# Performance work log

Hardware: AMD Instinct MI355X
Metric: run time of the kernel (lower is better)

The kernel has to match this reference:

```python
import jax, jax.numpy as jnp
import numpy as np

B, T, C = 128, 512, 1024  # batch, time (fixed by `line` buffer), channels


def fft_convolve(a, b):
    """Linear convolution via zero-padded FFT, sliced to a's length.
    a: (1, C, T) kernel, b: (B, C, T) signal. Returns (B, C, T)."""
    n = a.shape[-1]
    a_pad = jnp.pad(a, ((0, 0), (0, 0), (0, n)))
    b_pad = jnp.pad(b, ((0, 0), (0, 0), (0, n)))
    spec = jnp.fft.rfft(a_pad, axis=-1) * jnp.fft.rfft(b_pad, axis=-1)
    return jnp.fft.irfft(spec, n=2 * n, axis=-1)[..., :n]


def setup_inputs() -> dict:
    key = jax.random.key(0)
    k1, k2, k3, k4, k5 = jax.random.split(key, 5)
    bound = 1.0 / np.sqrt(C)  # nn.Linear default init range
    x = jax.random.normal(k1, (B, T, C), dtype=jnp.float32)
    W_proj = jax.random.uniform(k2, (C, C), jnp.float32, -bound, bound)
    W_values = jax.random.uniform(k3, (C, C), jnp.float32, -bound, bound)
    gain = jax.random.uniform(k4, (1, 1, C), jnp.float32, 0.01, 1.0)
    pow_ = jax.random.uniform(k5, (1, C, 1), jnp.float32, -6.0, 6.0)
    line = jnp.linspace(1.0, 0.0, T, dtype=jnp.float32)[None, None, :]  # (1,1,T)
    return {"x": x, "W_proj": W_proj, "W_values": W_values,
            "gain": gain, "pow_": pow_, "line": line}


def reference(x, W_proj, W_values, gain, pow_, line):
    # proj and values (bias-free Linears)
    h = jnp.einsum('btc,dc->btd', x, W_proj)          # (B,T,C)
    v = jnp.einsum('btc,dc->btd', h, W_values)        # (B,T,C)
    # learned power-law kernel, one decay per channel: (1,C,T)
    z = line ** (2.0 + jax.nn.sigmoid(pow_) * 100.0)
    # FFT long convolution along time
    y = fft_convolve(z, jnp.transpose(v, (0, 2, 1)))  # (B,C,T)
    y = jnp.transpose(y, (0, 2, 1))                    # (B,T,C)
    return jax.nn.relu(y * gain)
```

## Files before the change

kernel.cpp:

```cpp
#include <hip/hip_runtime.h>
#include <hip/hip_bf16.h>

#define B_ 128
#define T_ 512
#define C_ 1024

typedef __attribute__((ext_vector_type(8))) short short8;
typedef __attribute__((ext_vector_type(4))) float f32x4;

__device__ __forceinline__ unsigned short f2bf(float f){
  unsigned u; __builtin_memcpy(&u, &f, 4);
  u += 0x7FFFu + ((u >> 16) & 1u);
  return (unsigned short)(u >> 16);
}

typedef __attribute__((address_space(3))) unsigned lds_u32_t;
typedef __attribute__((address_space(1))) unsigned glb_u32_t;
typedef __attribute__((address_space(3))) char lds_char;
__device__ __forceinline__ void gload16(const void* g, void* l){
  __builtin_amdgcn_global_load_lds((const glb_u32_t*)g, (lds_u32_t*)l, 16, 0, 0);
}

__global__ void cast_f32_bf16(const float* __restrict__ in, unsigned short* __restrict__ out, long n){
  long i = (long)blockIdx.x * blockDim.x + threadIdx.x;
  long stride = (long)gridDim.x * blockDim.x;
  for (long j = i * 4; j < n; j += stride * 4){
    float4 v = *(const float4*)(in + j);
    ushort4 o; o.x = f2bf(v.x); o.y = f2bf(v.y); o.z = f2bf(v.z); o.w = f2bf(v.w);
    *(ushort4*)(out + j) = o;
  }
}

__global__ void transpose_cast(const float* __restrict__ in, unsigned short* __restrict__ out){
  __shared__ float tile[32][33];
  int c0 = blockIdx.x * 32, e0 = blockIdx.y * 32;
  int tx = threadIdx.x, ty = threadIdx.y;
  for (int r = 0; r < 32; r += 8)
    tile[ty + r][tx] = in[(size_t)(e0 + ty + r) * C_ + c0 + tx];
  __syncthreads();
  for (int r = 0; r < 32; r += 8)
    out[(size_t)(c0 + ty + r) * C_ + e0 + tx] = f2bf(tile[tx][ty + r]);
}

__global__ __launch_bounds__(256) void gemm_bt_bf16(
    const unsigned short* __restrict__ A,
    const unsigned short* __restrict__ Bt,
    unsigned short* __restrict__ Cc,
    int M, int N, int K)
{
  __shared__ short As[128 * 32];
  __shared__ short Bs[128 * 32];
  const int tid  = threadIdx.x;
  const int lane = tid & 63;
  const int wave = tid >> 6;
  const int wr = wave >> 1, wc = wave & 1;
  const int lr = lane & 15, kg = lane >> 4;
  const int m0 = blockIdx.x * 128;
  const int n0 = blockIdx.y * 128;

  f32x4 acc[4][4];
  #pragma unroll
  for (int mi = 0; mi < 4; mi++)
    #pragma unroll
    for (int ni = 0; ni < 4; ni++)
      acc[mi][ni] = (f32x4){0.f, 0.f, 0.f, 0.f};

  const int r1 = tid >> 2, ch1 = tid & 3;
  char* abase = (char*)As + (tid & ~63) * 16;
  char* bbase = (char*)Bs + (tid & ~63) * 16;

  for (int k0 = 0; k0 < K; k0 += 32){
    __syncthreads();
    gload16(A  + (size_t)(m0 + r1)      * K + k0 + ch1 * 8, abase);
    gload16(A  + (size_t)(m0 + 64 + r1) * K + k0 + ch1 * 8, abase + 4096);
    gload16(Bt + (size_t)(n0 + r1)      * K + k0 + ch1 * 8, bbase);
    gload16(Bt + (size_t)(n0 + 64 + r1) * K + k0 + ch1 * 8, bbase + 4096);
    __syncthreads();

    short8 af[4], bfr[4];
    #pragma unroll
    for (int mi = 0; mi < 4; mi++)
      af[mi] = *(const short8*)&As[(wr * 64 + mi * 16 + lr) * 32 + kg * 8];
    #pragma unroll
    for (int ni = 0; ni < 4; ni++)
      bfr[ni] = *(const short8*)&Bs[(wc * 64 + ni * 16 + lr) * 32 + kg * 8];
    #pragma unroll
    for (int mi = 0; mi < 4; mi++)
      #pragma unroll
      for (int ni = 0; ni < 4; ni++)
        acc[mi][ni] = __builtin_amdgcn_mfma_f32_16x16x32_bf16(af[mi], bfr[ni], acc[mi][ni], 0, 0, 0);
  }

  #pragma unroll
  for (int mi = 0; mi < 4; mi++)
    #pragma unroll
    for (int ni = 0; ni < 4; ni++){
      int n = n0 + wc * 64 + ni * 16 + lr;
      int mb = m0 + wr * 64 + mi * 16 + kg * 4;
      #pragma unroll
      for (int j = 0; j < 4; j++)
        Cc[(size_t)(mb + j) * N + n] = f2bf(acc[mi][ni][j]);
    }
}

#define SWZ(x) ((x) ^ ((((x) >> 7) & 3) << 4))

#define STAGE_A(kt, kh) { \
  int d_ = wv * 1024 + ln * 16; int o_ = SWZ(d_); \
  gload16(Ag + (size_t)(m0 + (o_ >> 6)) * 1024 + (kt) * 64 + (kh) * 32 + ((o_ >> 4) & 3) * 8, \
          ldsc + ((kt) & 1) * 32768 + (kh) * 16384 + wv * 1024); \
  d_ += 8192; o_ = SWZ(d_); \
  gload16(Ag + (size_t)(m0 + (o_ >> 6)) * 1024 + (kt) * 64 + (kh) * 32 + ((o_ >> 4) & 3) * 8, \
          ldsc + ((kt) & 1) * 32768 + (kh) * 16384 + 8192 + wv * 1024); }

#define STAGE_B(kt, kh) { \
  int d_ = wv * 1024 + ln * 16; int o_ = SWZ(d_); \
  gload16(Bg + (size_t)(n0 + (o_ >> 6)) * 1024 + (kt) * 64 + (kh) * 32 + ((o_ >> 4) & 3) * 8, \
          ldsc + 65536 + ((kt) & 1) * 32768 + (kh) * 16384 + wv * 1024); \
  d_ += 8192; o_ = SWZ(d_); \
  gload16(Bg + (size_t)(n0 + (o_ >> 6)) * 1024 + (kt) * 64 + (kh) * 32 + ((o_ >> 4) & 3) * 8, \
          ldsc + 65536 + ((kt) & 1) * 32768 + (kh) * 16384 + 8192 + wv * 1024); }

__global__ __launch_bounds__(512, 2) void gemm256_vt(
    const unsigned short* __restrict__ Ag,
    const unsigned short* __restrict__ Bg,
    unsigned short* __restrict__ vt)
{
  extern __shared__ char ldsc[];
  lds_char* lds3 = (lds_char*)ldsc;
  const int tid = threadIdx.x;
  const int ln  = tid & 63;
  const int wv  = tid >> 6;
  const int wr  = wv >> 2;
  const int wc  = wv & 3;
  const int lr  = ln & 15, kg = ln >> 4;
  const int id  = blockIdx.x;
  const int jj  = (id & 7) * 128 + (id >> 3);
  const int n0  = (jj & 3) * 256;
  const int m0  = (jj >> 2) * 256;

  f32x4 acc[8][4];
  #pragma unroll
  for (int mi = 0; mi < 8; mi++)
    #pragma unroll
    for (int ni = 0; ni < 4; ni++)
      acc[mi][ni] = (f32x4){0.f, 0.f, 0.f, 0.f};

  STAGE_A(0, 0); STAGE_A(0, 1); STAGE_B(0, 0); STAGE_B(0, 1);

  short8 af[2][8], bf2[2][4];

  #pragma unroll 1
  for (int t = 0; t < 16; ++t){
    const int S = t & 1;
    if (t < 15){
      STAGE_A(t + 1, 0); STAGE_A(t + 1, 1); STAGE_B(t + 1, 0); STAGE_B(t + 1, 1);
      __builtin_amdgcn_sched_barrier(0);
      asm volatile("s_waitcnt vmcnt(8)");
      __builtin_amdgcn_sched_barrier(0);
    } else {
      __builtin_amdgcn_sched_barrier(0);
      asm volatile("s_waitcnt vmcnt(0)");
      __builtin_amdgcn_sched_barrier(0);
    }
    __builtin_amdgcn_s_barrier();
    __builtin_amdgcn_sched_barrier(0);

    #pragma unroll
    for (int kk = 0; kk < 2; ++kk){
      #pragma unroll
      for (int mi = 0; mi < 8; mi++){
        int off = S * 32768 + kk * 16384 + (wr * 128 + mi * 16 + lr) * 64 + kg * 16;
        unsigned a_ = (unsigned)(size_t)(lds3 + SWZ(off));
        asm volatile("ds_read_b128 %0, %1" : "=v"(af[kk][mi]) : "v"(a_));
      }
      #pragma unroll
      for (int ni = 0; ni < 4; ni++){
        int off = 65536 + S * 32768 + kk * 16384 + (wc * 64 + ni * 16 + lr) * 64 + kg * 16;
        unsigned a_ = (unsigned)(size_t)(lds3 + SWZ(off));
        asm volatile("ds_read_b128 %0, %1" : "=v"(bf2[kk][ni]) : "v"(a_));
      }
    }

    asm volatile("s_waitcnt lgkmcnt(12)");
    __builtin_amdgcn_sched_barrier(0);
    __builtin_amdgcn_s_setprio(1);
    #pragma unroll
    for (int mi = 0; mi < 8; mi++)
      #pragma unroll
      for (int ni = 0; ni < 4; ni++)
        acc[mi][ni] = __builtin_amdgcn_mfma_f32_16x16x32_bf16(af[0][mi], bf2[0][ni], acc[mi][ni], 0, 0, 0);
    __builtin_amdgcn_s_setprio(0);

    asm volatile("s_waitcnt lgkmcnt(0)");
    __builtin_amdgcn_sched_barrier(0);
    __builtin_amdgcn_s_setprio(1);
    #pragma unroll
    for (int mi = 0; mi < 8; mi++)
      #pragma unroll
      for (int ni = 0; ni < 4; ni++)
        acc[mi][ni] = __builtin_amdgcn_mfma_f32_16x16x32_bf16(af[1][mi], bf2[1][ni], acc[mi][ni], 0, 0, 0);
    __builtin_amdgcn_s_setprio(0);
    __builtin_amdgcn_sched_barrier(0);
    __builtin_amdgcn_s_barrier();
  }

  #pragma unroll
  for (int mi = 0; mi < 8; mi++)
    #pragma unroll
    for (int ni = 0; ni < 4; ni++){
      int n  = n0 + wc * 64 + ni * 16 + lr;
      int mb = m0 + wr * 128 + mi * 16 + kg * 4;
      int bb = mb >> 9, t = mb & 511;
      ushort4 o;
      o.x = f2bf(acc[mi][ni][0]); o.y = f2bf(acc[mi][ni][1]);
      o.z = f2bf(acc[mi][ni][2]); o.w = f2bf(acc[mi][ni][3]);
      *(ushort4*)&vt[((size_t)n * B_ + bb) * T_ + t] = o;
    }
}

__global__ __launch_bounds__(256) void band_prep2(const float* __restrict__ pw,
                                                  const float* __restrict__ line,
                                                  unsigned short* __restrict__ band){
  __shared__ unsigned short zrow[64];
  const int c = blockIdx.x, d32 = blockIdx.y;
  const int tid = threadIdx.x;
  if (tid < 63){
    int k = d32 * 32 - 31 + tid;
    float z = 0.f;
    if (k >= 0 && k < T_){
      float p = pw[c];
      float e = 2.0f + 100.0f / (1.0f + expf(-p));
      float lv = line[k];
      z = (lv > 0.f) ? expf(e * logf(lv)) : 0.f;
    }
    zrow[tid] = f2bf(z);
  }
  __syncthreads();
  const size_t base = ((size_t)c * 16 + d32) * 1280;
  #pragma unroll
  for (int q = 0; q < 5; q++){
    int idx = tid + q * 256;
    int i = idx / 40, j = idx - i * 40;
    unsigned short v = 0;
    if (j < 32){
      int qq = i - j + 31;
      v = zrow[qq];
    }
    band[base + idx] = v;
  }
}

__global__ __launch_bounds__(256) void conv_mfma(
    const unsigned short* __restrict__ vt,
    const unsigned short* __restrict__ band,
    const float* __restrict__ gain,
    unsigned short* __restrict__ Ybf)
{
  __shared__ short Bs[128 * 32];
  __shared__ short Ab[16 * 1280];
  const int id  = blockIdx.x;
  const int xcd = id & 7;
  const int jj  = id >> 3;
  const int c   = xcd + ((jj >> 2) << 3);
  const int t0  = (jj & 3) << 7;
  const int tid = threadIdx.x, lane = tid & 63, wave = tid >> 6;
  const int wr = wave >> 1, wc = wave & 1, lr = lane & 15, kg = lane >> 4;
  const int K  = t0 + 128;
  const int nb = (t0 >> 5) + 4;

  {
    const unsigned short* src = band + (size_t)c * (16 * 1280);
    const int nch = nb * 160;
    for (int q0 = 0; q0 < nch; q0 += 256){
      int q = q0 + tid;
      char* dst = (char*)Ab + q0 * 16 + wave * 1024;
      if (q < nch) gload16(src + (size_t)q * 8, dst);
    }
  }

  f32x4 acc[4][4];
  #pragma unroll
  for (int mi = 0; mi < 4; mi++)
    #pragma unroll
    for (int ni = 0; ni < 4; ni++)
      acc[mi][ni] = (f32x4){0.f, 0.f, 0.f, 0.f};

  const int r1 = tid >> 2, ch1 = tid & 3;
  char* bbase = (char*)Bs + (tid & ~63) * 16;
  const size_t vbase = (size_t)c * B_ * T_;

  for (int k0 = 0; k0 < K; k0 += 32){
    __syncthreads();
    gload16(vt + vbase + (size_t)r1 * T_        + k0 + ch1 * 8, bbase);
    gload16(vt + vbase + (size_t)(64 + r1) * T_ + k0 + ch1 * 8, bbase + 4096);
    __syncthreads();

    short8 bfr[4];
    #pragma unroll
    for (int ni = 0; ni < 4; ni++)
      bfr[ni] = *(const short8*)&Bs[(wc * 64 + ni * 16 + lr) * 32 + kg * 8];

    const int dbase = ((t0 - k0) >> 5) + wr * 2;
    #pragma unroll
    for (int mi = 0; mi < 4; mi++){
      const int d32 = dbase + (mi >> 1);
      if (d32 >= 0){
        const int i = ((mi & 1) << 4) + lr;
        short8 af = *(const short8*)&Ab[d32 * 1280 + i * 40 + kg * 8];
        #pragma unroll
        for (int ni = 0; ni < 4; ni++)
          acc[mi][ni] = __builtin_amdgcn_mfma_f32_16x16x32_bf16(af, bfr[ni], acc[mi][ni], 0, 0, 0);
      }
    }
  }

  const float g = gain[c];
  #pragma unroll
  for (int mi = 0; mi < 4; mi++)
    #pragma unroll
    for (int ni = 0; ni < 4; ni++){
      int t = t0 + wr * 64 + mi * 16 + kg * 4;
      int b = wc * 64 + ni * 16 + lr;
      ushort4 o;
      o.x = f2bf(fmaxf(acc[mi][ni][0] * g, 0.f));
      o.y = f2bf(fmaxf(acc[mi][ni][1] * g, 0.f));
      o.z = f2bf(fmaxf(acc[mi][ni][2] * g, 0.f));
      o.w = f2bf(fmaxf(acc[mi][ni][3] * g, 0.f));
      *(ushort4*)&Ybf[((size_t)c * B_ + b) * T_ + t] = o;
    }
}

__global__ __launch_bounds__(256) void final_out(const unsigned short* __restrict__ Ybf,
                                                 float* __restrict__ out){
  __shared__ unsigned short tile[64][72];
  const int c0 = blockIdx.x * 64;
  const int t0 = blockIdx.y * 64;
  const int b  = blockIdx.z;
  const int tid = threadIdx.x;
  const int cr = tid >> 4;
  const int t4 = (tid & 15) * 4;
  for (int q = 0; q < 64; q += 16){
    ushort4 u = *(const ushort4*)&Ybf[((size_t)(c0 + cr + q) * B_ + b) * T_ + t0 + t4];
    *(ushort4*)&tile[cr + q][t4] = u;
  }
  __syncthreads();
  const int tr = tid >> 4;
  const int c4 = (tid & 15) * 4;
  for (int q = 0; q < 64; q += 16){
    int t = tr + q;
    float4 o;
    o.x = __uint_as_float((unsigned)tile[c4 + 0][t] << 16);
    o.y = __uint_as_float((unsigned)tile[c4 + 1][t] << 16);
    o.z = __uint_as_float((unsigned)tile[c4 + 2][t] << 16);
    o.w = __uint_as_float((unsigned)tile[c4 + 3][t] << 16);
    *(float4*)&out[((size_t)b * T_ + t0 + t) * C_ + c0 + c4] = o;
  }
}

extern "C" void kernel_launch(void* const* d_in, const int* in_sizes, int n_in,
                              void* d_out, int out_size, void* d_ws, size_t ws_size,
                              hipStream_t stream)
{
  (void)in_sizes; (void)n_in; (void)out_size; (void)ws_size;
  const float* x    = (const float*)d_in[0];
  const float* Wp   = (const float*)d_in[1];
  const float* Wv   = (const float*)d_in[2];
  const float* gain = (const float*)d_in[3];
  const float* pw   = (const float*)d_in[4];
  const float* line = (const float*)d_in[5];
  float* out = (float*)d_out;

  char* ws = (char*)d_ws;
  unsigned short* Ybf   = (unsigned short*)ws;
  unsigned short* WpT   = (unsigned short*)(ws + 134217728);
  unsigned short* Wv_bf = (unsigned short*)(ws + 134217728 + 2097152);
  unsigned short* W_f   = (unsigned short*)(ws + 134217728 + 2 * 2097152);
  unsigned short* x_bf  = (unsigned short*)d_out;
  unsigned short* vt    = (unsigned short*)d_out + 67108864;
  unsigned short* bandp = (unsigned short*)d_out;

  cast_f32_bf16<<<256, 256, 0, stream>>>(Wv, Wv_bf, (long)C_ * C_);
  transpose_cast<<<dim3(32, 32), dim3(32, 8), 0, stream>>>(Wp, WpT);
  gemm_bt_bf16<<<dim3(8, 8), 256, 0, stream>>>(Wv_bf, WpT, W_f, C_, C_, C_);
  cast_f32_bf16<<<2048, 256, 0, stream>>>(x, x_bf, (long)B_ * T_ * C_);
  gemm256_vt<<<1024, 512, 131072, stream>>>(x_bf, W_f, vt);
  band_prep2<<<dim3(1024, 16), 256, 0, stream>>>(pw, line, bandp);
  conv_mfma<<<4096, 256, 0, stream>>>(vt, bandp, gain, Ybf);
  final_out<<<dim3(16, 8, 128), 256, 0, stream>>>(Ybf, out);
}
```

Measured before the change: 522.2 us.

## Fuse fp32-to-bf16 cast of x into the main GEMM's A-tile loading

The separate cast kernel for x is removed. The big GEMM now loads fp32 x tiles into registers two steps ahead, converts them to bf16, and writes them to LDS with ds_write, while B is still staged through direct global-to-LDS loads. This saves one full pass writing and re-reading the 128 MB bf16 copy of x. In exchange the GEMM reads twice as many bytes for A, needs more registers, and has a more complex software pipeline in its main loop.

Result: slower. 678.0 us (+29.8%).

```diff
diff --git a/kernel.cpp b/kernel.cpp
--- a/kernel.cpp
+++ b/kernel.cpp
@@ -105,14 +105,6 @@
 
 #define SWZ(x) ((x) ^ ((((x) >> 7) & 3) << 4))
 
-#define STAGE_A(kt, kh) { \
-  int d_ = wv * 1024 + ln * 16; int o_ = SWZ(d_); \
-  gload16(Ag + (size_t)(m0 + (o_ >> 6)) * 1024 + (kt) * 64 + (kh) * 32 + ((o_ >> 4) & 3) * 8, \
-          ldsc + ((kt) & 1) * 32768 + (kh) * 16384 + wv * 1024); \
-  d_ += 8192; o_ = SWZ(d_); \
-  gload16(Ag + (size_t)(m0 + (o_ >> 6)) * 1024 + (kt) * 64 + (kh) * 32 + ((o_ >> 4) & 3) * 8, \
-          ldsc + ((kt) & 1) * 32768 + (kh) * 16384 + 8192 + wv * 1024); }
-
 #define STAGE_B(kt, kh) { \
   int d_ = wv * 1024 + ln * 16; int o_ = SWZ(d_); \
   gload16(Bg + (size_t)(n0 + (o_ >> 6)) * 1024 + (kt) * 64 + (kh) * 32 + ((o_ >> 4) & 3) * 8, \
@@ -121,8 +113,26 @@
   gload16(Bg + (size_t)(n0 + (o_ >> 6)) * 1024 + (kt) * 64 + (kh) * 32 + ((o_ >> 4) & 3) * 8, \
           ldsc + 65536 + ((kt) & 1) * 32768 + (kh) * 16384 + 8192 + wv * 1024); }
 
-__global__ __launch_bounds__(512, 2) void gemm256_vt(
-    const unsigned short* __restrict__ Ag,
+#define LOADA(kt) { \
+  _Pragma("unroll") for (int kh = 0; kh < 2; kh++) \
+    _Pragma("unroll") for (int hf = 0; hf < 2; hf++){ \
+      const float* p_ = Ag32 + (size_t)(m0 + rowA + hf * 128) * 1024 + (kt) * 64 + kh * 32 + c8 * 8; \
+      areg[kh][hf][0] = *(const float4*)p_; \
+      areg[kh][hf][1] = *(const float4*)(p_ + 4); } }
+
+#define CVTWRITE(slot) { \
+  _Pragma("unroll") for (int kh = 0; kh < 2; kh++) \
+    _Pragma("unroll") for (int hf = 0; hf < 2; hf++){ \
+      short8 w_; \
+      _Pragma("unroll") for (int q = 0; q < 4; q++){ \
+        w_[q]     = (short)f2bf(areg[kh][hf][0][q]); \
+        w_[q + 4] = (short)f2bf(areg[kh][hf][1][q]); } \
+      int d_ = wv * 1024 + ln * 16 + hf * 8192; \
+      unsigned ad_ = (unsigned)(size_t)(lds3 + (slot) * 32768 + kh * 16384 + SWZ(d_)); \
+      asm volatile("ds_write_b128 %0, %1" :: "v"(ad_), "v"(w_)); } }
+
+__global__ __launch_bounds__(512, 2) void gemm256_fused(
+    const float* __restrict__ Ag32,
     const unsigned short* __restrict__ Bg,
     unsigned short* __restrict__ vt)
 {
@@ -134,6 +144,8 @@
   const int wr  = wv >> 2;
   const int wc  = wv & 3;
   const int lr  = ln & 15, kg = ln >> 4;
+  const int rowA = wv * 16 + (ln >> 2);
+  const int c8   = ln & 3;
   const int id  = blockIdx.x;
   const int jj  = (id & 7) * 128 + (id >> 3);
   const int n0  = (jj & 3) * 256;
@@ -146,24 +158,28 @@
     for (int ni = 0; ni < 4; ni++)
       acc[mi][ni] = (f32x4){0.f, 0.f, 0.f, 0.f};
 
-  STAGE_A(0, 0); STAGE_A(0, 1); STAGE_B(0, 0); STAGE_B(0, 1);
+  float4 areg[2][2][2];
+
+  LOADA(0);
+  CVTWRITE(0);
+  __builtin_amdgcn_sched_barrier(0);
+  STAGE_B(0, 0); STAGE_B(0, 1);
+  __builtin_amdgcn_sched_barrier(0);
+  LOADA(1);
+  __builtin_amdgcn_sched_barrier(0);
+  asm volatile("s_waitcnt lgkmcnt(0)");
+  __builtin_amdgcn_sched_barrier(0);
+  asm volatile("s_waitcnt vmcnt(8)");
+  __builtin_amdgcn_sched_barrier(0);
+  __builtin_amdgcn_s_barrier();
 
   short8 af[2][8], bf2[2][4];
 
   #pragma unroll 1
   for (int t = 0; t < 16; ++t){
     const int S = t & 1;
-    if (t < 15){
-      STAGE_A(t + 1, 0); STAGE_A(t + 1, 1); STAGE_B(t + 1, 0); STAGE_B(t + 1, 1);
-      __builtin_amdgcn_sched_barrier(0);
-      asm volatile("s_waitcnt vmcnt(8)");
-      __builtin_amdgcn_sched_barrier(0);
-    } else {
-      __builtin_amdgcn_sched_barrier(0);
-      asm volatile("s_waitcnt vmcnt(0)");
-      __builtin_amdgcn_sched_barrier(0);
-    }
-    __builtin_amdgcn_s_barrier();
+
+    CVTWRITE(S ^ 1);
     __builtin_amdgcn_sched_barrier(0);
 
     #pragma unroll
@@ -181,6 +197,12 @@
         asm volatile("ds_read_b128 %0, %1" : "=v"(bf2[kk][ni]) : "v"(a_));
       }
     }
+    __builtin_amdgcn_sched_barrier(0);
+
+    if (t + 1 < 16) { STAGE_B(t + 1, 0); STAGE_B(t + 1, 1); }
+    __builtin_amdgcn_sched_barrier(0);
+    if (t < 14) { LOADA(t + 2); }
+    __builtin_amdgcn_sched_barrier(0);
 
     asm volatile("s_waitcnt lgkmcnt(12)");
     __builtin_amdgcn_sched_barrier(0);
@@ -201,6 +223,10 @@
       for (int ni = 0; ni < 4; ni++)
         acc[mi][ni] = __builtin_amdgcn_mfma_f32_16x16x32_bf16(af[1][mi], bf2[1][ni], acc[mi][ni], 0, 0, 0);
     __builtin_amdgcn_s_setprio(0);
+    __builtin_amdgcn_sched_barrier(0);
+
+    if (t < 14) { asm volatile("s_waitcnt vmcnt(8)"); }
+    else        { asm volatile("s_waitcnt vmcnt(0)"); }
     __builtin_amdgcn_sched_barrier(0);
     __builtin_amdgcn_s_barrier();
   }
@@ -376,15 +402,13 @@
   unsigned short* WpT   = (unsigned short*)(ws + 134217728);
   unsigned short* Wv_bf = (unsigned short*)(ws + 134217728 + 2097152);
   unsigned short* W_f   = (unsigned short*)(ws + 134217728 + 2 * 2097152);
-  unsigned short* x_bf  = (unsigned short*)d_out;
   unsigned short* vt    = (unsigned short*)d_out + 67108864;
   unsigned short* bandp = (unsigned short*)d_out;
 
   cast_f32_bf16<<<256, 256, 0, stream>>>(Wv, Wv_bf, (long)C_ * C_);
   transpose_cast<<<dim3(32, 32), dim3(32, 8), 0, stream>>>(Wp, WpT);
   gemm_bt_bf16<<<dim3(8, 8), 256, 0, stream>>>(Wv_bf, WpT, W_f, C_, C_, C_);
-  cast_f32_bf16<<<2048, 256, 0, stream>>>(x, x_bf, (long)B_ * T_ * C_);
-  gemm256_vt<<<1024, 512, 131072, stream>>>(x_bf, W_f, vt);
+  gemm256_fused<<<1024, 512, 131072, stream>>>(x, W_f, vt);
   band_prep2<<<dim3(1024, 16), 256, 0, stream>>>(pw, line, bandp);
   conv_mfma<<<4096, 256, 0, stream>>>(vt, bandp, gain, Ybf);
   final_out<<<dim3(16, 8, 128), 256, 0, stream>>>(Ybf, out);
```
